# Performance work log

Measured on AMD Instinct MI355X. Metric: run time of the kernel, lower is better.

## Reference

```python
import jax, jax.numpy as jnp
import numpy as np

B, T, S, D = 4, 16, 256, 1024
H, HKV = 16, 4
HD = D // H  # 64
N_IMG = 240  # image tokens; remaining S-N_IMG are agent tokens
LOGIT_CAP = 50.0
EPS = 1e-6


def _build_mask():
    # modality-aware mask: image tokens see only image tokens; agent tokens see all
    m = np.zeros((S, S), dtype=bool)
    m[:N_IMG, :N_IMG] = True
    m[N_IMG:, :] = True
    return jnp.asarray(m)


def _build_rope(s, hd):
    half = hd // 2
    inv_freq = 1.0 / (10000.0 ** (np.arange(half, dtype=np.float32) / half))
    pos = np.arange(s, dtype=np.float32)
    ang = np.outer(pos, inv_freq)  # (S, hd/2)
    return jnp.asarray(np.cos(ang)), jnp.asarray(np.sin(ang))


def setup_inputs() -> dict:
    key = jax.random.key(0)
    ks = jax.random.split(key, 7)
    rope_cos, rope_sin = _build_rope(S, HD)
    sc = 0.02
    return {
        "x": jax.random.normal(ks[0], (B, T, S, D), jnp.float32),
        "attn_mask": _build_mask(),
        "rope_cos": rope_cos,
        "rope_sin": rope_sin,
        "Wq": jax.random.normal(ks[1], (D, H * HD), jnp.float32) * sc,
        "Wk": jax.random.normal(ks[2], (D, HKV * HD), jnp.float32) * sc,
        "Wv": jax.random.normal(ks[3], (D, HKV * HD), jnp.float32) * sc,
        "Wo": jax.random.normal(ks[4], (D, D), jnp.float32) * sc,
        "q_scale": jnp.ones((HD,), jnp.float32),
        "k_scale": jnp.ones((HD,), jnp.float32),
    }


def _rmsnorm(t, scale):
    # RMSNorm over head_dim
    var = jnp.mean(jnp.square(t), axis=-1, keepdims=True)
    return t * jax.lax.rsqrt(var + EPS) * scale


def _rope(t, cos, sin):
    # rotate-half RoPE; t: (N, S, h, hd), cos/sin: (S, hd/2)
    half = t.shape[-1] // 2
    t1, t2 = t[..., :half], t[..., half:]
    c = cos[None, :, None, :]
    s = sin[None, :, None, :]
    return jnp.concatenate([t1 * c - t2 * s, t2 * c + t1 * s], axis=-1)


def reference(x, attn_mask, rope_cos, rope_sin, Wq, Wk, Wv, Wo, q_scale, k_scale):
    b, t, s, d = x.shape
    n = b * t
    xf = x.reshape(n, s, d)
    q = (xf @ Wq).reshape(n, s, H, HD)
    k = (xf @ Wk).reshape(n, s, HKV, HD)
    v = (xf @ Wv).reshape(n, s, HKV, HD)
    # QK-norm then RoPE
    q = _rope(_rmsnorm(q, q_scale), rope_cos, rope_sin)
    k = _rope(_rmsnorm(k, k_scale), rope_cos, rope_sin)
    # GQA: repeat kv heads
    rep = H // HKV
    k = jnp.repeat(k, rep, axis=2)
    v = jnp.repeat(v, rep, axis=2)
    scale = 1.0 / jnp.sqrt(jnp.asarray(HD, x.dtype))
    scores = jnp.einsum('nqhd,nkhd->nhqk', q, k) * scale
    # logit soft-capping
    scores = LOGIT_CAP * jnp.tanh(scores / LOGIT_CAP)
    big_neg = jnp.asarray(jnp.finfo(scores.dtype).min, scores.dtype)
    scores = jnp.where(attn_mask[None, None], scores, big_neg)
    p = jax.nn.softmax(scores, axis=-1)
    out = jnp.einsum('nhqk,nkhd->nqhd', p, v).reshape(n, s, d)
    return (out @ Wo).reshape(b, t, s, d)
```

## Files before the change

### kernel.cpp

```cpp
#include <hip/hip_runtime.h>

typedef __bf16 v8bf __attribute__((ext_vector_type(8)));
typedef __bf16 v4bf __attribute__((ext_vector_type(4)));
typedef float floatx4 __attribute__((ext_vector_type(4)));

#define MFMA16(a, b, c) __builtin_amdgcn_mfma_f32_16x16x32_bf16(a, b, c, 0, 0, 0)
#define GLL16(gp, lp)                                                        \
    __builtin_amdgcn_global_load_lds(                                        \
        (const __attribute__((address_space(1))) void*)(gp),                 \
        (__attribute__((address_space(3))) void*)(lp), 16, 0, 0)
#define VMW(n) asm volatile("s_waitcnt vmcnt(" #n ")" ::: "memory")
#define BARRIER() asm volatile("s_barrier" ::: "memory")

__global__ void cast_x(const float* __restrict__ x, __bf16* __restrict__ xb, int n4) {
    int i = blockIdx.x * blockDim.x + threadIdx.x;
    int stride = gridDim.x * blockDim.x;
    for (; i < n4; i += stride) {
        float4 v = ((const float4*)x)[i];
        v4bf o;
        o[0] = (__bf16)v.x; o[1] = (__bf16)v.y; o[2] = (__bf16)v.z; o[3] = (__bf16)v.w;
        ((v4bf*)xb)[i] = o;
    }
}

__global__ void transW(const float* __restrict__ W0, const float* __restrict__ W1,
                       const float* __restrict__ W2, const float* __restrict__ W3,
                       __bf16* __restrict__ dqkv, __bf16* __restrict__ dwo) {
    __shared__ __bf16 tile[64][65];
    int k0 = blockIdx.x * 64;
    int byy = blockIdx.y;
    bool isO = byy >= 24;
    int c0 = (isO ? byy - 24 : byy) * 64;
    for (int i = threadIdx.x; i < 4096; i += 256) {
        int k = i >> 6, c = i & 63;
        int gc = c0 + c;
        float v;
        if (isO)            v = W3[(k0 + k) * 1024 + gc];
        else if (gc < 1024) v = W0[(k0 + k) * 1024 + gc];
        else if (gc < 1280) v = W1[(k0 + k) * 256 + gc - 1024];
        else                v = W2[(k0 + k) * 256 + gc - 1280];
        tile[c][k] = (__bf16)v;
    }
    __syncthreads();
    __bf16* dst = isO ? dwo : dqkv;
    for (int i = threadIdx.x; i < 4096; i += 256) {
        int c = i >> 6, k = i & 63;
        dst[(c0 + c) * 1024 + k0 + k] = tile[c][k];
    }
}

template <int BM, typename OUT>
__global__ __launch_bounds__(512, 2) void gemm_bt(const __bf16* __restrict__ A,
                                                  const __bf16* __restrict__ B,
                                                  OUT* __restrict__ C, int N) {
    constexpr int MF = BM / 32;
    constexpr int SLAB = (BM + 256) * 32;
    __shared__ __attribute__((aligned(16))) __bf16 smem[4 * SLAB];
    const int t = threadIdx.x, lane = t & 63, w = t >> 6;
    const int gx = gridDim.x;
    const int nwg = gx * gridDim.y;
    const int id = blockIdx.y * gx + blockIdx.x;
    const int swz = (id & 7) * (nwg >> 3) + (id >> 3);
    const int m0 = (swz / gx) * BM, n0 = (swz % gx) * 256;
    const int wm = (w >> 2) * (BM / 2), wn = (w & 3) * 64;
    const int rl = lane >> 2;
    const int gl = (lane & 3) ^ ((lane >> 3) & 3);
    const __bf16* pA = A + (long)(m0 + w * (BM / 8) + rl) * 1024 + gl * 8;
    const __bf16* pB = B + (long)(n0 + w * 32 + rl) * 1024 + gl * 8;
    const int lr = lane & 15, quad = lane >> 4, m = lane & 15;
    const int ga = ((quad ^ ((lr >> 1) & 3)) * 8);
    floatx4 acc[MF][4] = {};

    auto STAGE = [&](int s) {
        __bf16* base = smem + (s & 3) * SLAB;
        const __bf16* sa = pA + s * 32;
        const __bf16* sb = pB + s * 32;
        if constexpr (BM == 256) {
            GLL16(sa, base + w * 1024);
            GLL16(sa + 16 * 1024, base + w * 1024 + 512);
        } else {
            GLL16(sa, base + w * 512);
        }
        __bf16* bb = base + BM * 32;
        GLL16(sb, bb + w * 1024);
        GLL16(sb + 16 * 1024, bb + w * 1024 + 512);
    };
    auto COMPUTE = [&](int s) {
        const __bf16* As_ = smem + (s & 3) * SLAB;
        const __bf16* Bs_ = As_ + BM * 32;
        v8bf af[MF], bq[4];
#pragma unroll
        for (int i = 0; i < MF; ++i)
            af[i] = *(const v8bf*)(As_ + (wm + i * 16 + lr) * 32 + ga);
#pragma unroll
        for (int j = 0; j < 4; ++j)
            bq[j] = *(const v8bf*)(Bs_ + (wn + j * 16 + lr) * 32 + ga);
        __builtin_amdgcn_s_setprio(1);
#pragma unroll
        for (int i = 0; i < MF; ++i)
#pragma unroll
            for (int j = 0; j < 4; ++j)
                acc[i][j] = MFMA16(af[i], bq[j], acc[i][j]);
        __builtin_amdgcn_s_setprio(0);
    };

    STAGE(0); STAGE(1); STAGE(2);
#pragma unroll 1
    for (int s = 0; s < 29; ++s) {
        STAGE(s + 3);
        if constexpr (BM == 256) VMW(12); else VMW(9);
        BARRIER();
        COMPUTE(s);
        BARRIER();
    }
    if constexpr (BM == 256) VMW(8); else VMW(6);
    BARRIER(); COMPUTE(29); BARRIER();
    if constexpr (BM == 256) VMW(4); else VMW(3);
    BARRIER(); COMPUTE(30); BARRIER();
    VMW(0);
    BARRIER(); COMPUTE(31);
    __syncthreads();

    const int row2 = lane >> 2, cb = lane & 3;
    if constexpr (sizeof(OUT) == 2) {
        __bf16* tile = smem + w * (16 * 68);
#pragma unroll
        for (int i = 0; i < MF; ++i) {
#pragma unroll
            for (int j = 0; j < 4; ++j)
#pragma unroll
                for (int r = 0; r < 4; ++r)
                    tile[(quad * 4 + r) * 68 + j * 16 + m] = (__bf16)acc[i][j][r];
            __bf16* dst = (__bf16*)C + (long)(m0 + wm + i * 16 + row2) * N + n0 + wn + cb * 16;
            *(v8bf*)dst = *(const v8bf*)(&tile[row2 * 68 + cb * 16]);
            *(v8bf*)(dst + 8) = *(const v8bf*)(&tile[row2 * 68 + cb * 16 + 8]);
        }
    } else {
        float* tile = (float*)smem + w * (16 * 66);
#pragma unroll
        for (int i = 0; i < MF; ++i) {
#pragma unroll
            for (int j = 0; j < 4; ++j)
#pragma unroll
                for (int r = 0; r < 4; ++r)
                    tile[(quad * 4 + r) * 66 + j * 16 + m] = acc[i][j][r];
            float* dst = (float*)C + (long)(m0 + wm + i * 16 + row2) * N + n0 + wn + cb * 16;
#pragma unroll
            for (int c = 0; c < 4; ++c)
                *(floatx4*)(dst + c * 4) = *(const floatx4*)(&tile[row2 * 66 + cb * 16 + c * 4]);
        }
    }
}

__global__ __launch_bounds__(256) void knorm(const __bf16* __restrict__ qkv,
                                             const float* __restrict__ rc,
                                             const float* __restrict__ rs,
                                             const float* __restrict__ ksc,
                                             __bf16* __restrict__ Kb) {
    int item = blockIdx.x * 4 + (threadIdx.x >> 6);
    int lane = threadIdx.x & 63;
    int row = item >> 2, hk = item & 3;
    int n = row >> 8, s = row & 255;
    float v = (float)qkv[(long)row * 1536 + 1024 + hk * 64 + lane];
    float sq = v * v;
#pragma unroll
    for (int msk = 1; msk < 64; msk <<= 1) sq += __shfl_xor(sq, msk);
    float rr = rsqrtf(sq * (1.f / 64.f) + 1e-6f);
    v = v * rr * ksc[lane];
    float c = rc[s * 32 + (lane & 31)];
    float sn = rs[s * 32 + (lane & 31)];
    float p = __shfl_xor(v, 32);
    v = (lane < 32) ? (v * c - p * sn) : (v * c + p * sn);
    Kb[((long)((n * 4 + hk) * 256 + s) << 6) + lane] = (__bf16)v;
}

__global__ __launch_bounds__(512) void attn_kernel(const __bf16* __restrict__ qkv,
                                                   const __bf16* __restrict__ Kb,
                                                   const float* __restrict__ rc,
                                                   const float* __restrict__ rs,
                                                   const float* __restrict__ qsc,
                                                   __bf16* __restrict__ O) {
    __shared__ __attribute__((aligned(16))) __bf16 KV[256 * 64];
    __shared__ __attribute__((aligned(16))) __bf16 Ps[8][16][40];
    const int bx = blockIdx.x;
    const int n = bx >> 5, h = (bx >> 1) & 15, half = bx & 1, hk = h >> 2;
    const int t = threadIdx.x, lane = t & 63, w = t >> 6;
    const int m = lane & 15, quad = lane >> 4;

    for (int p = 0; p < 4; ++p) {
        int l = t + p * 512;
        int s = l >> 3, cg = l & 7;
        v8bf kv = *(const v8bf*)(Kb + ((long)((n * 4 + hk) * 256 + s) << 6) + cg * 8);
        *(v8bf*)(&KV[s * 64 + ((cg ^ (s & 7)) * 8)]) = kv;
    }
    const int srow = half * 128 + w * 16 + m;
    const __bf16* qp = qkv + (long)(n * 256 + srow) * 1536 + h * 64 + quad * 8;
    v8bf qr0 = *(const v8bf*)(qp);
    v8bf qr1 = *(const v8bf*)(qp + 32);
    float f0[8], f1[8], ss = 0.f;
#pragma unroll
    for (int j = 0; j < 8; ++j) {
        f0[j] = (float)qr0[j]; f1[j] = (float)qr1[j];
        ss += f0[j] * f0[j] + f1[j] * f1[j];
    }
    ss += __shfl_xor(ss, 16);
    ss += __shfl_xor(ss, 32);
    float rr = rsqrtf(ss * (1.f / 64.f) + 1e-6f);
    v8bf qa0, qa1;
#pragma unroll
    for (int j = 0; j < 8; ++j) {
        int hd = quad * 8 + j;
        float t1 = f0[j] * rr * qsc[hd];
        float t2 = f1[j] * rr * qsc[32 + hd];
        float c = rc[srow * 32 + hd], sn = rs[srow * 32 + hd];
        qa0[j] = (__bf16)(t1 * c - t2 * sn);
        qa1[j] = (__bf16)(t2 * c + t1 * sn);
    }
    __syncthreads();

    floatx4 sc[16];
#pragma unroll
    for (int ti = 0; ti < 16; ++ti) {
        int kr = ti * 16 + m;
        v8bf b0 = *(const v8bf*)(&KV[kr * 64 + ((quad ^ (kr & 7)) * 8)]);
        v8bf b1 = *(const v8bf*)(&KV[kr * 64 + (((quad + 4) ^ (kr & 7)) * 8)]);
        floatx4 a = {0.f, 0.f, 0.f, 0.f};
        a = MFMA16(qa0, b0, a);
        a = MFMA16(qa1, b1, a);
        sc[ti] = a;
    }

    const int qbase = half * 128 + w * 16 + quad * 4;
    float sum[4] = {0.f, 0.f, 0.f, 0.f};
#pragma unroll
    for (int ti = 0; ti < 16; ++ti)
#pragma unroll
        for (int r = 0; r < 4; ++r) {
            float v = sc[ti][r];
            float e = __builtin_amdgcn_exp2f(v * 0.0072134752f);
            float capped = 50.f - 100.f * __builtin_amdgcn_rcpf(e + 1.f);
            float p = __builtin_amdgcn_exp2f(capped * 1.44269504f);
            if (ti == 15 && (qbase + r) < 240) p = 0.f;
            sc[ti][r] = p;
            sum[r] += p;
        }
    float inv[4];
#pragma unroll
    for (int r = 0; r < 4; ++r) {
#pragma unroll
        for (int msk = 1; msk < 16; msk <<= 1) sum[r] += __shfl_xor(sum[r], msk);
        inv[r] = __builtin_amdgcn_rcpf(sum[r]);
    }

    __syncthreads();
    for (int p = 0; p < 4; ++p) {
        int l = t + p * 512;
        int s = l >> 3, cg = l & 7;
        v8bf vv = *(const v8bf*)(qkv + (long)(n * 256 + s) * 1536 + 1280 + hk * 64 + cg * 8);
#pragma unroll
        for (int j = 0; j < 8; ++j)
            KV[(cg * 8 + j) * 256 + ((s >> 3) ^ j) * 8 + (s & 7)] = vv[j];
    }
    __syncthreads();

    floatx4 oacc[4] = {};
#pragma unroll
    for (int kc = 0; kc < 8; ++kc) {
#pragma unroll
        for (int ht = 0; ht < 2; ++ht) {
            int ti = kc * 2 + ht;
#pragma unroll
            for (int r = 0; r < 4; ++r)
                Ps[w][quad * 4 + r][ht * 16 + m] = (__bf16)sc[ti][r];
        }
        v8bf pa = *(const v8bf*)(&Ps[w][m][quad * 8]);
#pragma unroll
        for (int ct = 0; ct < 4; ++ct) {
            int hd = ct * 16 + m;
            int sg = kc * 4 + quad;
            v8bf vb = *(const v8bf*)(&KV[hd * 256 + ((sg ^ (hd & 7)) * 8)]);
            oacc[ct] = MFMA16(pa, vb, oacc[ct]);
        }
    }
#pragma unroll
    for (int ct = 0; ct < 4; ++ct)
#pragma unroll
        for (int r = 0; r < 4; ++r) {
            int qrow = half * 128 + w * 16 + quad * 4 + r;
            O[(long)(n * 256 + qrow) * 1024 + h * 64 + ct * 16 + m] =
                (__bf16)(oacc[ct][r] * inv[r]);
        }
}

extern "C" void kernel_launch(void* const* d_in, const int* in_sizes, int n_in,
                              void* d_out, int out_size, void* d_ws, size_t ws_size,
                              hipStream_t stream) {
    const float* x  = (const float*)d_in[0];
    const float* rc = (const float*)d_in[2];
    const float* rs = (const float*)d_in[3];
    const float* Wq = (const float*)d_in[4];
    const float* Wk = (const float*)d_in[5];
    const float* Wv = (const float*)d_in[6];
    const float* Wo = (const float*)d_in[7];
    const float* qs = (const float*)d_in[8];
    const float* ks = (const float*)d_in[9];
    float* out = (float*)d_out;
    char* ws = (char*)d_ws;

    __bf16* x_bf    = (__bf16*)(ws);
    __bf16* WqkvT   = (__bf16*)(ws + (32l << 20));
    __bf16* WoT     = (__bf16*)(ws + (35l << 20));
    __bf16* qkv_bf  = (__bf16*)(ws + (37l << 20));
    __bf16* K_bf    = (__bf16*)(ws + (85l << 20));
    __bf16* attn_bf = (__bf16*)(ws + (93l << 20));

    cast_x<<<4096, 256, 0, stream>>>(x, x_bf, 16777216 / 4);
    transW<<<dim3(16, 40), 256, 0, stream>>>(Wq, Wk, Wv, Wo, WqkvT, WoT);
    gemm_bt<256, __bf16><<<dim3(6, 64), 512, 0, stream>>>(x_bf, WqkvT, qkv_bf, 1536);
    knorm<<<16384, 256, 0, stream>>>(qkv_bf, rc, rs, ks, K_bf);
    attn_kernel<<<2048, 512, 0, stream>>>(qkv_bf, K_bf, rc, rs, qs, attn_bf);
    gemm_bt<256, float><<<dim3(4, 64), 512, 0, stream>>>(attn_bf, WoT, out, 1024);
}
```

Before: 324.0 us.

## Retile GEMM to 128x256 tiles with 4 waves and triple-buffered LDS

Both projection GEMMs move from 256x256 tiles with 8 waves and 4-stage LDS buffering to 128x256 tiles with 4 waves, each wave computing a 128x64 output slab, and 3-stage buffering. The grid doubles in the M direction, giving more workgroups to spread over the compute units and a smaller LDS footprint that may allow more resident blocks. In exchange, each wave holds twice as many accumulators, which raises register pressure. The shallower pipeline may also expose more global load latency.

```diff
diff --git a/kernel.cpp b/kernel.cpp
--- a/kernel.cpp
+++ b/kernel.cpp
@@ -49,102 +49,95 @@
     }
 }
 
-template <int BM, typename OUT>
-__global__ __launch_bounds__(512, 2) void gemm_bt(const __bf16* __restrict__ A,
+template <typename OUT>
+__global__ __launch_bounds__(256, 2) void gemm_bt(const __bf16* __restrict__ A,
                                                   const __bf16* __restrict__ B,
                                                   OUT* __restrict__ C, int N) {
-    constexpr int MF = BM / 32;
-    constexpr int SLAB = (BM + 256) * 32;
-    __shared__ __attribute__((aligned(16))) __bf16 smem[4 * SLAB];
+    constexpr int SLAB = (128 + 256) * 32;
+    __shared__ __attribute__((aligned(16))) __bf16 smem[3 * SLAB];
     const int t = threadIdx.x, lane = t & 63, w = t >> 6;
     const int gx = gridDim.x;
     const int nwg = gx * gridDim.y;
     const int id = blockIdx.y * gx + blockIdx.x;
     const int swz = (id & 7) * (nwg >> 3) + (id >> 3);
-    const int m0 = (swz / gx) * BM, n0 = (swz % gx) * 256;
-    const int wm = (w >> 2) * (BM / 2), wn = (w & 3) * 64;
+    const int m0 = (swz / gx) * 128, n0 = (swz % gx) * 256;
+    const int wn = w * 64;
     const int rl = lane >> 2;
     const int gl = (lane & 3) ^ ((lane >> 3) & 3);
-    const __bf16* pA = A + (long)(m0 + w * (BM / 8) + rl) * 1024 + gl * 8;
-    const __bf16* pB = B + (long)(n0 + w * 32 + rl) * 1024 + gl * 8;
+    const __bf16* pA = A + (long)(m0 + w * 32 + rl) * 1024 + gl * 8;
+    const __bf16* pB = B + (long)(n0 + w * 64 + rl) * 1024 + gl * 8;
     const int lr = lane & 15, quad = lane >> 4, m = lane & 15;
     const int ga = ((quad ^ ((lr >> 1) & 3)) * 8);
-    floatx4 acc[MF][4] = {};
+    floatx4 acc[8][4] = {};
 
     auto STAGE = [&](int s) {
-        __bf16* base = smem + (s & 3) * SLAB;
+        __bf16* base = smem + (s % 3) * SLAB;
         const __bf16* sa = pA + s * 32;
         const __bf16* sb = pB + s * 32;
-        if constexpr (BM == 256) {
-            GLL16(sa, base + w * 1024);
-            GLL16(sa + 16 * 1024, base + w * 1024 + 512);
-        } else {
-            GLL16(sa, base + w * 512);
-        }
-        __bf16* bb = base + BM * 32;
-        GLL16(sb, bb + w * 1024);
-        GLL16(sb + 16 * 1024, bb + w * 1024 + 512);
+        GLL16(sa,             base + w * 1024);
+        GLL16(sa + 16 * 1024, base + w * 1024 + 512);
+        __bf16* bb = base + 4096;
+        GLL16(sb,             bb + w * 2048);
+        GLL16(sb + 16 * 1024, bb + w * 2048 + 512);
+        GLL16(sb + 32 * 1024, bb + w * 2048 + 1024);
+        GLL16(sb + 48 * 1024, bb + w * 2048 + 1536);
     };
     auto COMPUTE = [&](int s) {
-        const __bf16* As_ = smem + (s & 3) * SLAB;
-        const __bf16* Bs_ = As_ + BM * 32;
-        v8bf af[MF], bq[4];
-#pragma unroll
-        for (int i = 0; i < MF; ++i)
-            af[i] = *(const v8bf*)(As_ + (wm + i * 16 + lr) * 32 + ga);
+        const __bf16* As_ = smem + (s % 3) * SLAB;
+        const __bf16* Bs_ = As_ + 4096;
+        v8bf af[8], bq[4];
+#pragma unroll
+        for (int i = 0; i < 8; ++i)
+            af[i] = *(const v8bf*)(As_ + (i * 16 + lr) * 32 + ga);
 #pragma unroll
         for (int j = 0; j < 4; ++j)
             bq[j] = *(const v8bf*)(Bs_ + (wn + j * 16 + lr) * 32 + ga);
         __builtin_amdgcn_s_setprio(1);
 #pragma unroll
-        for (int i = 0; i < MF; ++i)
+        for (int i = 0; i < 8; ++i)
 #pragma unroll
             for (int j = 0; j < 4; ++j)
                 acc[i][j] = MFMA16(af[i], bq[j], acc[i][j]);
         __builtin_amdgcn_s_setprio(0);
     };
 
-    STAGE(0); STAGE(1); STAGE(2);
+    STAGE(0); STAGE(1);
 #pragma unroll 1
-    for (int s = 0; s < 29; ++s) {
-        STAGE(s + 3);
-        if constexpr (BM == 256) VMW(12); else VMW(9);
+    for (int s = 0; s < 30; ++s) {
+        STAGE(s + 2);
+        VMW(12);
         BARRIER();
         COMPUTE(s);
         BARRIER();
     }
-    if constexpr (BM == 256) VMW(8); else VMW(6);
-    BARRIER(); COMPUTE(29); BARRIER();
-    if constexpr (BM == 256) VMW(4); else VMW(3);
-    BARRIER(); COMPUTE(30); BARRIER();
-    VMW(0);
-    BARRIER(); COMPUTE(31);
+    VMW(6);  BARRIER(); COMPUTE(30); BARRIER();
+    VMW(0);  BARRIER(); COMPUTE(31);
     __syncthreads();
 
     const int row2 = lane >> 2, cb = lane & 3;
     if constexpr (sizeof(OUT) == 2) {
         __bf16* tile = smem + w * (16 * 68);
 #pragma unroll
-        for (int i = 0; i < MF; ++i) {
+        for (int i = 0; i < 8; ++i) {
 #pragma unroll
             for (int j = 0; j < 4; ++j)
 #pragma unroll
                 for (int r = 0; r < 4; ++r)
                     tile[(quad * 4 + r) * 68 + j * 16 + m] = (__bf16)acc[i][j][r];
-            __bf16* dst = (__bf16*)C + (long)(m0 + wm + i * 16 + row2) * N + n0 + wn + cb * 16;
+            __bf16* dst = (__bf16*)C + (long)(m0 + i * 16 + row2) * N + n0 + wn + cb * 16;
             *(v8bf*)dst = *(const v8bf*)(&tile[row2 * 68 + cb * 16]);
             *(v8bf*)(dst + 8) = *(const v8bf*)(&tile[row2 * 68 + cb * 16 + 8]);
         }
     } else {
         float* tile = (float*)smem + w * (16 * 66);
 #pragma unroll
-        for (int i = 0; i < MF; ++i) {
+        for (int i = 0; i < 8; ++i) {
 #pragma unroll
             for (int j = 0; j < 4; ++j)
 #pragma unroll
                 for (int r = 0; r < 4; ++r)
                     tile[(quad * 4 + r) * 66 + j * 16 + m] = acc[i][j][r];
-            float* dst = (float*)C + (long)(m0 + wm + i * 16 + row2) * N + n0 + wn + cb * 16;
+            float* dst = (float*)C + (long)(m0 + i * 16 + row2) * N + n0 + wn + cb * 16;
 #pragma unroll
             for (int c = 0; c < 4; ++c)
                 *(floatx4*)(dst + c * 4) = *(const floatx4*)(&tile[row2 * 66 + cb * 16 + c * 4]);
@@ -316,8 +309,8 @@
 
     cast_x<<<4096, 256, 0, stream>>>(x, x_bf, 16777216 / 4);
     transW<<<dim3(16, 40), 256, 0, stream>>>(Wq, Wk, Wv, Wo, WqkvT, WoT);
-    gemm_bt<256, __bf16><<<dim3(6, 64), 512, 0, stream>>>(x_bf, WqkvT, qkv_bf, 1536);
+    gemm_bt<__bf16><<<dim3(6, 128), 256, 0, stream>>>(x_bf, WqkvT, qkv_bf, 1536);
     knorm<<<16384, 256, 0, stream>>>(qkv_bf, rc, rs, ks, K_bf);
     attn_kernel<<<2048, 512, 0, stream>>>(qkv_bf, K_bf, rc, rs, qs, attn_bf);
-    gemm_bt<256, float><<<dim3(4, 64), 512, 0, stream>>>(attn_bf, WoT, out, 1024);
-}
+    gemm_bt<float><<<dim3(4, 128), 256, 0, stream>>>(attn_bf, WoT, out, 1024);
+}
```

Result: faster. 313.8 us (-3.1%).
